# Kernel optimization log

Hardware: AMD Instinct MI355X
Metric: run time of the kernel (lower is better)

The kernel has to match this reference:

```python
import jax, jax.numpy as jnp
import numpy as np

EPS = 1e-5
NUM_CLASSES = 8

def _conv(x, w, b):
    # reflect pad 1 then valid 3x3 conv, NCHW / OIHW
    x = jnp.pad(x, ((0, 0), (0, 0), (1, 1), (1, 1)), mode='reflect')
    y = jax.lax.conv_general_dilated(x, w, (1, 1), 'VALID',
        dimension_numbers=('NCHW', 'OIHW', 'NCHW'))
    return y + b[None, :, None, None]

def _up2(x):
    B, C, H, W = x.shape
    return jax.image.resize(x, (B, C, 2 * H, 2 * W), method='bilinear')

def _nearest_resize_seg(seg, H, W):
    # torch F.interpolate mode='nearest': src = floor(dst * in / out)
    ih = jnp.arange(H) * seg.shape[2] // H
    iw = jnp.arange(W) * seg.shape[3] // W
    return seg[:, :, ih][:, :, :, iw]

def _seg_norm(x, seg):
    # per-class InstanceNorm2d (no affine) on masked copies, summed
    H, W = x.shape[2], x.shape[3]
    seg_r = _nearest_resize_seg(seg, H, W)  # [B,1,H,W]
    out = jnp.zeros_like(x)
    for c in range(NUM_CLASSES):
        mask = (seg_r == c).astype(x.dtype)
        xc = x * mask
        mu = jnp.mean(xc, axis=(2, 3), keepdims=True)
        var = jnp.mean(xc * xc, axis=(2, 3), keepdims=True) - mu * mu
        out = out + (xc - mu) * jax.lax.rsqrt(var + EPS)
    return out

def setup_inputs() -> dict:
    key = jax.random.key(0)
    ks = jax.random.split(key, 24)
    d = {}
    d['x'] = jax.random.normal(ks[0], (4, 512, 64, 64), dtype=jnp.float32)
    d['seg_map'] = jax.random.randint(ks[1], (4, 1, 64, 64), 0, NUM_CLASSES, dtype=jnp.int32)
    shapes = [(256, 512), (256, 256), (256, 256), (256, 256), (128, 256),
              (128, 128), (64, 128), (64, 64), (3, 64)]
    names = ['1', '2', '3', '4', '5', '6', '7', '8', 'f']
    for i, ((o, ic), nm) in enumerate(zip(shapes, names)):
        fan_in = ic * 9
        bound = 1.0 / np.sqrt(fan_in)
        d['w' + nm] = jax.random.uniform(ks[2 + 2 * i], (o, ic, 3, 3), jnp.float32, -bound, bound)
        d['b' + nm] = jax.random.uniform(ks[3 + 2 * i], (o,), jnp.float32, -bound, bound)
    return d

def reference(x, seg_map, w1, b1, w2, b2, w3, b3, w4, b4, w5, b5,
              w6, b6, w7, b7, w8, b8, wf, bf):
    h = jax.nn.relu(_conv(x, w1, b1))
    h = _seg_norm(h, seg_map)
    h = _up2(h)
    h = jax.nn.relu(_conv(h, w2, b2))
    h = jax.nn.relu(_conv(h, w3, b3))
    h = jax.nn.relu(_conv(h, w4, b4))
    h = jax.nn.relu(_conv(h, w5, b5))
    h = _seg_norm(h, seg_map)
    h = _up2(h)
    h = jax.nn.relu(_conv(h, w6, b6))
    h = jax.nn.relu(_conv(h, w7, b7))
    h = _seg_norm(h, seg_map)
    h = _up2(h)
    h = jax.nn.relu(_conv(h, w8, b8))
    return _conv(h, wf, bf)
```

## Files before the change

kernel.cpp:

```cpp
#include <hip/hip_runtime.h>

typedef unsigned int uint;
typedef unsigned short ushort;
typedef __bf16 bf16x8 __attribute__((ext_vector_type(8)));
typedef float f32x4 __attribute__((ext_vector_type(4)));
typedef uint u32x4 __attribute__((ext_vector_type(4)));
typedef ushort u16x4 __attribute__((ext_vector_type(4)));

__device__ __forceinline__ float bf_lo(uint u) { return __builtin_bit_cast(float, u << 16); }
__device__ __forceinline__ float bf_hi(uint u) { return __builtin_bit_cast(float, u & 0xFFFF0000u); }
__device__ __forceinline__ ushort f2bf(float f) {
  uint u = __builtin_bit_cast(uint, f);
  return (ushort)((u + 0x7FFFu + ((u >> 16) & 1u)) >> 16);
}

template<int NCH, int ROWS, int RELU>
__global__ __launch_bounds__(256) void conv_mfma_k(
    const ushort* __restrict__ in, const ushort* __restrict__ wp,
    const float* __restrict__ bias, ushort* __restrict__ out,
    int Cout, int H, int W,
    int in_row0, int in_rows, int out_row0, int out_rows,
    int ob_row0, int ob_rows) {
  constexpr int Cin = NCH * 32;
  constexpr int SLOTS = (ROWS + 2) * 66 * 4;
  constexpr int NPASS = (SLOTS + 255) / 256;
  constexpr int LAST = SLOTS - (NPASS - 1) * 256;
  __shared__ ushort lds[2][SLOTS * 8];
  const int tid = threadIdx.x;
  const int lane = tid & 63;
  const int wv = tid >> 6;
  const int wx0 = blockIdx.x * 64;
  const int nCoB = Cout >> 6;
  const int cob = (blockIdx.z % nCoB) * 64;
  const int b = blockIdx.z / nCoB;
  const int h0 = out_row0 + blockIdx.y * ROWS;
  const int nCb = Cout >> 4;
  const int cb0 = cob >> 4;

  int hs[ROWS + 2];
#pragma unroll
  for (int r = 0; r < ROWS + 2; ++r) {
    int hh = h0 - 1 + r;
    if (hh < 0) hh = 1;
    if (hh >= H) hh = 2 * (H - 1) - hh;
    hh = min(max(hh, in_row0), in_row0 + in_rows - 1);
    hs[r] = hh - in_row0;
  }

  const ushort* gsrc[NPASS];
  uint lof[NPASS];
#pragma unroll
  for (int p = 0; p < NPASS; ++p) {
    const int t = p * 256 + tid;
    const int px_g = t >> 2, kgs = t & 3;
    int rr = px_g / 66;
    int px = px_g - rr * 66;
    if (rr > ROWS + 1) { px = px_g - (ROWS + 2) * 66; rr = ROWS + 1; }
    const int kg = kgs ^ ((px >> 1) & 3);
    int wsrc = wx0 + px - 1;
    wsrc = (wsrc < 0) ? 1 : (wsrc >= W ? W - 2 : wsrc);
    gsrc[p] = in + ((size_t)(b * in_rows + hs[rr]) * W + wsrc) * Cin + kg * 8;
    lof[p] = (uint)((p * 256 + wv * 64) * 8);
  }

  const int bpx = wv * 16 + (lane & 15);
  const int bkg = lane >> 4;

  f32x4 acc[ROWS][4] = {};

  auto stage = [&](int buf, int ci0) {
#pragma unroll
    for (int p = 0; p < NPASS; ++p) {
      if (p + 1 < NPASS || tid < LAST)
        __builtin_amdgcn_global_load_lds(
            (const __attribute__((address_space(1))) void*)(gsrc[p] + ci0),
            (__attribute__((address_space(3))) void*)(&lds[buf][lof[p]]), 16, 0, 0);
    }
  };
  auto compute = [&](int buf, int kc) {
    const ushort* lb = &lds[buf][0];
#pragma unroll
    for (int t9 = 0; t9 < 9; ++t9) {
      const int dr = t9 / 3, s = t9 - dr * 3;
      bf16x8 afr[4];
#pragma unroll
      for (int ii = 0; ii < 4; ++ii) {
        const int off = (((t9 * nCb + cb0 + ii) * NCH + kc) << 9) + (lane << 3);
        afr[ii] = __builtin_bit_cast(bf16x8, *(const u32x4*)(wp + off));
      }
      const int px = bpx + s;
      const int swz = bkg ^ ((px >> 1) & 3);
#pragma unroll
      for (int rr = 0; rr < ROWS; ++rr) {
        const int sl = (((rr + dr) * 66 + px) << 2) + swz;
        const bf16x8 bfrag = __builtin_bit_cast(bf16x8, *(const u32x4*)(lb + sl * 8));
#pragma unroll
        for (int ii = 0; ii < 4; ++ii)
          acc[rr][ii] = __builtin_amdgcn_mfma_f32_16x16x32_bf16(afr[ii], bfrag, acc[rr][ii], 0, 0, 0);
      }
    }
  };

  stage(0, 0);
  asm volatile("s_waitcnt vmcnt(0)" ::: "memory");
  __syncthreads();
#pragma unroll 1
  for (int c = 0; c < NCH; ++c) {
    if (c + 1 < NCH) stage((c + 1) & 1, (c + 1) * 32);
    compute(c & 1, c);
    asm volatile("s_waitcnt vmcnt(0)" ::: "memory");
    __syncthreads();
  }

  const int cofr = cob + (lane >> 4) * 4;
  const int pxo = wx0 + bpx;
#pragma unroll
  for (int rr = 0; rr < ROWS; ++rr) {
    const int h = h0 + rr;
    if (h >= out_row0 + out_rows) break;
    const size_t base = ((size_t)(b * ob_rows + (h - ob_row0)) * W + pxo) * Cout;
#pragma unroll
    for (int ii = 0; ii < 4; ++ii) {
      u16x4 pk;
#pragma unroll
      for (int g = 0; g < 4; ++g) {
        float v = acc[rr][ii][g] + bias[cofr + ii * 16 + g];
        if (RELU) v = fmaxf(v, 0.f);
        pk[g] = f2bf(v);
      }
      *(u16x4*)(out + base + cofr + ii * 16) = pk;
    }
  }
}

__global__ __launch_bounds__(256) void convf_mfma_k(
    const ushort* __restrict__ in, const ushort* __restrict__ wp,
    const float* __restrict__ bias, float* __restrict__ out,
    int in_row0, int in_rows, int out_row0, int out_rows) {
  constexpr int ROWS = 4, NCH = 2, W = 512, H = 512, Cin = 64;
  constexpr int SLOTS = (ROWS + 2) * 66 * 4;
  constexpr int NPASS = (SLOTS + 255) / 256;
  constexpr int LAST = SLOTS - (NPASS - 1) * 256;
  __shared__ ushort lds[2][SLOTS * 8];
  const int tid = threadIdx.x;
  const int lane = tid & 63;
  const int wv = tid >> 6;
  const int wx0 = blockIdx.x * 64;
  const int b = blockIdx.z;
  const int h0 = out_row0 + blockIdx.y * ROWS;

  int hs[ROWS + 2];
#pragma unroll
  for (int r = 0; r < ROWS + 2; ++r) {
    int hh = h0 - 1 + r;
    if (hh < 0) hh = 1;
    if (hh >= H) hh = 2 * (H - 1) - hh;
    hh = min(max(hh, in_row0), in_row0 + in_rows - 1);
    hs[r] = hh - in_row0;
  }
  const ushort* gsrc[NPASS];
  uint lof[NPASS];
#pragma unroll
  for (int p = 0; p < NPASS; ++p) {
    const int t = p * 256 + tid;
    const int px_g = t >> 2, kgs = t & 3;
    int rr = px_g / 66;
    int px = px_g - rr * 66;
    if (rr > ROWS + 1) { px = px_g - (ROWS + 2) * 66; rr = ROWS + 1; }
    const int kg = kgs ^ ((px >> 1) & 3);
    int wsrc = wx0 + px - 1;
    wsrc = (wsrc < 0) ? 1 : (wsrc >= W ? W - 2 : wsrc);
    gsrc[p] = in + ((size_t)(b * in_rows + hs[rr]) * W + wsrc) * Cin + kg * 8;
    lof[p] = (uint)((p * 256 + wv * 64) * 8);
  }
  const int bpx = wv * 16 + (lane & 15);
  const int bkg = lane >> 4;
  f32x4 acc[ROWS] = {};

  auto stage = [&](int buf, int ci0) {
#pragma unroll
    for (int p = 0; p < NPASS; ++p) {
      if (p + 1 < NPASS || tid < LAST)
        __builtin_amdgcn_global_load_lds(
            (const __attribute__((address_space(1))) void*)(gsrc[p] + ci0),
            (__attribute__((address_space(3))) void*)(&lds[buf][lof[p]]), 16, 0, 0);
    }
  };
  auto compute = [&](int buf, int kc) {
    const ushort* lb = &lds[buf][0];
#pragma unroll
    for (int t9 = 0; t9 < 9; ++t9) {
      const int dr = t9 / 3, s = t9 - dr * 3;
      const int off = (((t9 * NCH) + kc) << 9) + (lane << 3);
      const bf16x8 afr = __builtin_bit_cast(bf16x8, *(const u32x4*)(wp + off));
      const int px = bpx + s;
      const int swz = bkg ^ ((px >> 1) & 3);
#pragma unroll
      for (int rr = 0; rr < ROWS; ++rr) {
        const int sl = (((rr + dr) * 66 + px) << 2) + swz;
        const bf16x8 bfrag = __builtin_bit_cast(bf16x8, *(const u32x4*)(lb + sl * 8));
        acc[rr] = __builtin_amdgcn_mfma_f32_16x16x32_bf16(afr, bfrag, acc[rr], 0, 0, 0);
      }
    }
  };

  stage(0, 0);
  asm volatile("s_waitcnt vmcnt(0)" ::: "memory");
  __syncthreads();
#pragma unroll 1
  for (int c = 0; c < NCH; ++c) {
    if (c + 1 < NCH) stage((c + 1) & 1, (c + 1) * 32);
    compute(c & 1, c);
    asm volatile("s_waitcnt vmcnt(0)" ::: "memory");
    __syncthreads();
  }

  if ((lane >> 4) == 0) {
    const int pxo = wx0 + bpx;
#pragma unroll
    for (int rr = 0; rr < ROWS; ++rr) {
      const int h = h0 + rr;
      if (h >= out_row0 + out_rows) break;
#pragma unroll
      for (int g = 0; g < 3; ++g)
        out[(((size_t)(b * 3 + g)) << 18) + ((size_t)h << 9) + pxo] = acc[rr][g] + bias[g];
    }
  }
}

__global__ __launch_bounds__(256) void sn_sum_k(
    const ushort* __restrict__ x, const int* __restrict__ seg,
    float* __restrict__ Ssum, float* __restrict__ Qsum, int C, int logW, int nsl) {
  const int W = 1 << logW, sh = logW - 6;
  const int b = blockIdx.x / nsl, sl = blockIdx.x % nsl;
  const int PPT = 256 / C;
  const int c = threadIdx.x % C;
  const int sub = threadIdx.x / C;
  const int rows = W / nsl;
  const int p0 = sl * rows * W;
  const int np = rows * W;
  const ushort* xp = x + ((size_t)b << (2 * logW)) * C + (size_t)p0 * C;
  const int* segb = seg + (b << 12);
  float S[8] = {0, 0, 0, 0, 0, 0, 0, 0};
  float Q[8] = {0, 0, 0, 0, 0, 0, 0, 0};
  for (int k = sub; k < np; k += PPT) {
    const int p = p0 + k;
    const int cls = segb[(((p >> logW) >> sh) << 6) + ((p & (W - 1)) >> sh)];
    const uint u = xp[(size_t)k * C + c];
    const float v = __builtin_bit_cast(float, u << 16);
#pragma unroll
    for (int t = 0; t < 8; ++t) {
      const bool m = (cls == t);
      S[t] += m ? v : 0.f;
      Q[t] += m ? v * v : 0.f;
    }
  }
#pragma unroll
  for (int t = 0; t < 8; ++t) {
    atomicAdd(&Ssum[((b << 3) + t) * C + c], S[t]);
    atomicAdd(&Qsum[((b << 3) + t) * C + c], Q[t]);
  }
}

__global__ void sn_fin_k(const float* __restrict__ Ssum, const float* __restrict__ Qsum,
                         float* __restrict__ RS, float* __restrict__ KK, int C, float invN) {
  const int tid = threadIdx.x;
  const int b = tid / C, c = tid % C;
  float K = 0.f;
#pragma unroll
  for (int t = 0; t < 8; ++t) {
    const float s = Ssum[((b << 3) + t) * C + c];
    const float q = Qsum[((b << 3) + t) * C + c];
    const float mu = s * invN;
    const float var = q * invN - mu * mu;
    const float r = rsqrtf(var + 1e-5f);
    RS[((b << 3) + t) * C + c] = r;
    K += mu * r;
  }
  KK[b * C + c] = K;
}

__global__ __launch_bounds__(256) void up2norm_k(
    const ushort* __restrict__ src, const int* __restrict__ seg,
    const float* __restrict__ RS, const float* __restrict__ KK,
    ushort* __restrict__ out, int C, int logWs, int out_row0, int out_rows) {
  const int Ws = 1 << logWs, W2 = Ws << 1, sh = logWs - 6;
  const int cpb = C >> 3;
  int i = blockIdx.x * 256 + threadIdx.x;
  const int total = 4 * out_rows * W2 * cpb;
  if (i >= total) return;
  const int cc = (i % cpb) * 8; i /= cpb;
  const int ow = i % W2; i /= W2;
  const int r = i % out_rows;
  const int b = i / out_rows;
  const int oh = out_row0 + r;

  int hl = (oh - 1) >> 1;
  const float hf = (oh & 1) ? 0.25f : 0.75f;
  const int hh = min(hl + 1, Ws - 1);
  hl = max(hl, 0);
  int wl = (ow - 1) >> 1;
  const float wfc = (ow & 1) ? 0.25f : 0.75f;
  const int wh = min(wl + 1, Ws - 1);
  wl = max(wl, 0);

  const size_t pl = (size_t)b << (2 * logWs);
  const u32x4 xll = *(const u32x4*)(src + ((pl + hl * Ws + wl) * C + cc));
  const u32x4 xlh = *(const u32x4*)(src + ((pl + hl * Ws + wh) * C + cc));
  const u32x4 xhl = *(const u32x4*)(src + ((pl + hh * Ws + wl) * C + cc));
  const u32x4 xhh = *(const u32x4*)(src + ((pl + hh * Ws + wh) * C + cc));
  const int* segb = seg + (b << 12);
  const int cll = segb[((hl >> sh) << 6) + (wl >> sh)];
  const int clh = segb[((hl >> sh) << 6) + (wh >> sh)];
  const int chl = segb[((hh >> sh) << 6) + (wl >> sh)];
  const int chh = segb[((hh >> sh) << 6) + (wh >> sh)];
  const float* rll = RS + ((b << 3) + cll) * C + cc;
  const float* rlh = RS + ((b << 3) + clh) * C + cc;
  const float* rhl = RS + ((b << 3) + chl) * C + cc;
  const float* rhh = RS + ((b << 3) + chh) * C + cc;
  const float* kk = KK + b * C + cc;

  u32x4 res;
#pragma unroll
  for (int q = 0; q < 4; ++q) {
    const int c0 = 2 * q, c1 = 2 * q + 1;
    const float na0 = bf_lo(xll[q]) * rll[c0], nb0 = bf_lo(xlh[q]) * rlh[c0];
    const float nc0 = bf_lo(xhl[q]) * rhl[c0], nd0 = bf_lo(xhh[q]) * rhh[c0];
    const float na1 = bf_hi(xll[q]) * rll[c1], nb1 = bf_hi(xlh[q]) * rlh[c1];
    const float nc1 = bf_hi(xhl[q]) * rhl[c1], nd1 = bf_hi(xhh[q]) * rhh[c1];
    const float t0 = na0 + wfc * (nb0 - na0), bo0 = nc0 + wfc * (nd0 - nc0);
    const float t1 = na1 + wfc * (nb1 - na1), bo1 = nc1 + wfc * (nd1 - nc1);
    const float o0 = t0 + hf * (bo0 - t0) - kk[c0];
    const float o1 = t1 + hf * (bo1 - t1) - kk[c1];
    res[q] = (uint)f2bf(o0) | ((uint)f2bf(o1) << 16);
  }
  *(u32x4*)(out + (((size_t)(b * out_rows + r)) * W2 + ow) * C + cc) = res;
}

__global__ __launch_bounds__(256) void packw_k(const float* __restrict__ w,
                                               ushort* __restrict__ wp, int Co, int Ci) {
  const int i = blockIdx.x * 256 + threadIdx.x;
  const int tot = Co * Ci * 9;
  if (i >= tot) return;
  const int nKc = Ci >> 5;
  const int nCb = Co >> 4;
  const int j = i & 7;
  const int l = (i >> 3) & 63;
  int rest = i >> 9;
  const int kc = rest % nKc; rest /= nKc;
  const int cb = rest % nCb;
  const int t9 = rest / nCb;
  const int co = cb * 16 + (l & 15);
  const int ci = kc * 32 + (l >> 4) * 8 + j;
  wp[i] = f2bf(w[((size_t)(co * Ci + ci)) * 9 + t9]);
}

__global__ __launch_bounds__(256) void packwf_k(const float* __restrict__ w,
                                                ushort* __restrict__ wp) {
  const int i = blockIdx.x * 256 + threadIdx.x;
  if (i >= 9216) return;
  const int j = i & 7;
  const int l = (i >> 3) & 63;
  const int rest = i >> 9;
  const int kc = rest & 1;
  const int t9 = rest >> 1;
  const int co = l & 15;
  const int ci = kc * 32 + (l >> 4) * 8 + j;
  wp[i] = (co < 3) ? f2bf(w[((size_t)(co * 64 + ci)) * 9 + t9]) : (ushort)0;
}

__global__ __launch_bounds__(256) void cvt_x_k(const float* __restrict__ x,
                                               ushort* __restrict__ xn) {
  __shared__ float tile[32][65];
  const int p0 = blockIdx.x * 64, c0 = blockIdx.y * 32, b = blockIdx.z;
  for (int k = threadIdx.x; k < 2048; k += 256) {
    const int ci = k >> 6, pj = k & 63;
    tile[ci][pj] = x[(((size_t)(b * 512 + c0 + ci)) << 12) + p0 + pj];
  }
  __syncthreads();
  for (int k = threadIdx.x; k < 2048; k += 256) {
    const int ci = k & 31, pj = k >> 5;
    xn[((((size_t)b << 12) + p0 + pj)) * 512 + c0 + ci] = f2bf(tile[ci][pj]);
  }
}

extern "C" void kernel_launch(void* const* d_in, const int* in_sizes, int n_in,
                              void* d_out, int out_size, void* d_ws, size_t ws_size,
                              hipStream_t stream) {
  const float* x = (const float*)d_in[0];
  const int* seg = (const int*)d_in[1];
  const float *w1 = (const float*)d_in[2], *b1 = (const float*)d_in[3];
  const float *w2 = (const float*)d_in[4], *b2 = (const float*)d_in[5];
  const float *w3 = (const float*)d_in[6], *b3 = (const float*)d_in[7];
  const float *w4 = (const float*)d_in[8], *b4 = (const float*)d_in[9];
  const float *w5 = (const float*)d_in[10], *b5 = (const float*)d_in[11];
  const float *w6 = (const float*)d_in[12], *b6 = (const float*)d_in[13];
  const float *w7 = (const float*)d_in[14], *b7 = (const float*)d_in[15];
  const float *w8 = (const float*)d_in[16], *b8 = (const float*)d_in[17];
  const float *wf = (const float*)d_in[18], *bf = (const float*)d_in[19];
  float* outp = (float*)d_out;

  char* wsb = (char*)d_ws;
  const size_t MB = 1048576;
  ushort* w1p = (ushort*)(wsb + 0);
  ushort* w2p = (ushort*)(wsb + 2359296);
  ushort* w3p = (ushort*)(wsb + 3538944);
  ushort* w4p = (ushort*)(wsb + 4718592);
  ushort* w5p = (ushort*)(wsb + 5898240);
  ushort* w6p = (ushort*)(wsb + 6488064);
  ushort* w7p = (ushort*)(wsb + 6782976);
  ushort* w8p = (ushort*)(wsb + 6930432);
  ushort* wfp = (ushort*)(wsb + 7004160);
  float* Ssum = (float*)(wsb + 8388608);
  float* Qsum = (float*)(wsb + 8421376);
  float* RS = (float*)(wsb + 8454144);
  float* KK = (float*)(wsb + 8486912);
  ushort* XN = (ushort*)(wsb + 9 * MB);
  ushort* A1 = (ushort*)(wsb + 25 * MB);
  ushort* U1 = (ushort*)(wsb + 33 * MB);
  ushort* C2 = (ushort*)(wsb + 65 * MB);
  ushort* C3 = (ushort*)(wsb + 9 * MB);
  ushort* C4 = (ushort*)(wsb + 41 * MB);
  ushort* C5 = (ushort*)(wsb + 9 * MB);
  ushort* U6 = (ushort*)(wsb + 25 * MB);
  ushort* C6 = (ushort*)(wsb + 58 * MB);
  ushort* C7 = (ushort*)(wsb + 91 * MB);
  ushort* U8 = (ushort*)(wsb + 9 * MB);
  ushort* C8 = (ushort*)(wsb + 43 * MB);

  auto cdiv = [](int a, int b) { return (a + b - 1) / b; };

  cvt_x_k<<<dim3(64, 16, 4), 256, 0, stream>>>(x, XN);
  packw_k<<<cdiv(1179648, 256), 256, 0, stream>>>(w1, w1p, 256, 512);
  packw_k<<<cdiv(589824, 256), 256, 0, stream>>>(w2, w2p, 256, 256);
  packw_k<<<cdiv(589824, 256), 256, 0, stream>>>(w3, w3p, 256, 256);
  packw_k<<<cdiv(589824, 256), 256, 0, stream>>>(w4, w4p, 256, 256);
  packw_k<<<cdiv(294912, 256), 256, 0, stream>>>(w5, w5p, 128, 256);
  packw_k<<<cdiv(147456, 256), 256, 0, stream>>>(w6, w6p, 128, 128);
  packw_k<<<cdiv(73728, 256), 256, 0, stream>>>(w7, w7p, 64, 128);
  packw_k<<<cdiv(36864, 256), 256, 0, stream>>>(w8, w8p, 64, 64);
  packwf_k<<<36, 256, 0, stream>>>(wf, wfp);

  conv_mfma_k<16, 2, 1><<<dim3(1, 32, 16), 256, 0, stream>>>(
      XN, w1p, b1, A1, 256, 64, 64, 0, 64, 0, 64, 0, 64);
  hipMemsetAsync(Ssum, 0, 65536, stream);
  sn_sum_k<<<4 * 32, 256, 0, stream>>>(A1, seg, Ssum, Qsum, 256, 6, 32);
  sn_fin_k<<<1, 1024, 0, stream>>>(Ssum, Qsum, RS, KK, 256, 1.f / 4096.f);
  up2norm_k<<<cdiv(4 * 128 * 128 * 32, 256), 256, 0, stream>>>(A1, seg, RS, KK, U1, 256, 6, 0, 128);

  conv_mfma_k<8, 4, 1><<<dim3(2, 32, 16), 256, 0, stream>>>(
      U1, w2p, b2, C2, 256, 128, 128, 0, 128, 0, 128, 0, 128);
  conv_mfma_k<8, 4, 1><<<dim3(2, 32, 16), 256, 0, stream>>>(
      C2, w3p, b3, C3, 256, 128, 128, 0, 128, 0, 128, 0, 128);
  conv_mfma_k<8, 4, 1><<<dim3(2, 32, 16), 256, 0, stream>>>(
      C3, w4p, b4, C4, 256, 128, 128, 0, 128, 0, 128, 0, 128);
  conv_mfma_k<8, 4, 1><<<dim3(2, 32, 8), 256, 0, stream>>>(
      C4, w5p, b5, C5, 128, 128, 128, 0, 128, 0, 128, 0, 128);
  hipMemsetAsync(Ssum, 0, 65536, stream);
  sn_sum_k<<<4 * 64, 256, 0, stream>>>(C5, seg, Ssum, Qsum, 128, 7, 64);
  sn_fin_k<<<1, 512, 0, stream>>>(Ssum, Qsum, RS, KK, 128, 1.f / 16384.f);

  for (int kb = 0; kb < 2; ++kb) {
    const int r0 = kb * 128;
    const int Rlo = max(r0 - 1, 0), Rhi = min(r0 + 128, 255);
    const int rows6 = Rhi - Rlo + 1;
    const int Ulo = max(Rlo - 1, 0), Uhi = min(Rhi + 1, 255);
    const int rowsU = Uhi - Ulo + 1;
    up2norm_k<<<cdiv(4 * rowsU * 256 * 16, 256), 256, 0, stream>>>(C5, seg, RS, KK, U6, 128, 7, Ulo, rowsU);
    conv_mfma_k<4, 4, 1><<<dim3(4, cdiv(rows6, 4), 8), 256, 0, stream>>>(
        U6, w6p, b6, C6, 128, 256, 256, Ulo, rowsU, Rlo, rows6, Rlo, rows6);
    conv_mfma_k<4, 4, 1><<<dim3(4, 32, 4), 256, 0, stream>>>(
        C6, w7p, b7, C7, 64, 256, 256, Rlo, rows6, r0, 128, 0, 256);
  }
  hipMemsetAsync(Ssum, 0, 65536, stream);
  sn_sum_k<<<4 * 128, 256, 0, stream>>>(C7, seg, Ssum, Qsum, 64, 8, 128);
  sn_fin_k<<<1, 256, 0, stream>>>(Ssum, Qsum, RS, KK, 64, 1.f / 65536.f);

  for (int kb = 0; kb < 4; ++kb) {
    const int r0 = kb * 128;
    const int Rlo = max(r0 - 1, 0), Rhi = min(r0 + 128, 511);
    const int rows8 = Rhi - Rlo + 1;
    const int Ulo = max(Rlo - 1, 0), Uhi = min(Rhi + 1, 511);
    const int rowsU = Uhi - Ulo + 1;
    up2norm_k<<<cdiv(4 * rowsU * 512 * 8, 256), 256, 0, stream>>>(C7, seg, RS, KK, U8, 64, 8, Ulo, rowsU);
    conv_mfma_k<2, 4, 1><<<dim3(8, cdiv(rows8, 4), 4), 256, 0, stream>>>(
        U8, w8p, b8, C8, 64, 512, 512, Ulo, rowsU, Rlo, rows8, Rlo, rows8);
    convf_mfma_k<<<dim3(8, 32, 4), 256, 0, stream>>>(C8, wfp, bf, outp, Rlo, rows8, r0, 128);
  }
}
```

Before: 1.228 ms.

## Software-pipeline conv fragment loads across taps and merge weight packing launches

Inside the MFMA conv kernels, the weight and LDS fragments for the next 3x3 tap are loaded into a second register buffer while MFMAs run on the current tap. The global-to-LDS staging of the next channel chunk is now issued after compute instead of before it. The eight weight-packing launches are merged into one kernel that walks a segment table. Together these aim to hide load latency and cut launch overhead, but the double buffering raises register use, and issuing the stage after compute shortens the window in which that global load can overlap with MFMA work.

```diff
diff --git a/kernel.cpp b/kernel.cpp
--- a/kernel.cpp
+++ b/kernel.cpp
@@ -79,24 +79,40 @@
   };
   auto compute = [&](int buf, int kc) {
     const ushort* lb = &lds[buf][0];
+    u32x4 afr[2][4];
+    u32x4 bfr[2][ROWS];
+#pragma unroll
+    for (int ii = 0; ii < 4; ++ii)
+      afr[0][ii] = *(const u32x4*)(wp + ((((0 * nCb + cb0 + ii) * NCH + kc) << 9) + (lane << 3)));
+    {
+      const int px = bpx;
+      const int swz = bkg ^ ((px >> 1) & 3);
+#pragma unroll
+      for (int rr = 0; rr < ROWS; ++rr)
+        bfr[0][rr] = *(const u32x4*)(lb + (((rr * 66 + px) << 2) + swz) * 8);
+    }
 #pragma unroll
     for (int t9 = 0; t9 < 9; ++t9) {
-      const int dr = t9 / 3, s = t9 - dr * 3;
-      bf16x8 afr[4];
-#pragma unroll
-      for (int ii = 0; ii < 4; ++ii) {
-        const int off = (((t9 * nCb + cb0 + ii) * NCH + kc) << 9) + (lane << 3);
-        afr[ii] = __builtin_bit_cast(bf16x8, *(const u32x4*)(wp + off));
+      const int cur = t9 & 1, nxt = cur ^ 1;
+      if (t9 < 8) {
+        const int tn = t9 + 1;
+        const int drn = tn / 3, sn = tn - drn * 3;
+#pragma unroll
+        for (int ii = 0; ii < 4; ++ii)
+          afr[nxt][ii] = *(const u32x4*)(wp + ((((tn * nCb + cb0 + ii) * NCH + kc) << 9) + (lane << 3)));
+        const int pxn = bpx + sn;
+        const int swzn = bkg ^ ((pxn >> 1) & 3);
+#pragma unroll
+        for (int rr = 0; rr < ROWS; ++rr)
+          bfr[nxt][rr] = *(const u32x4*)(lb + ((((rr + drn) * 66 + pxn) << 2) + swzn) * 8);
       }
-      const int px = bpx + s;
-      const int swz = bkg ^ ((px >> 1) & 3);
 #pragma unroll
       for (int rr = 0; rr < ROWS; ++rr) {
-        const int sl = (((rr + dr) * 66 + px) << 2) + swz;
-        const bf16x8 bfrag = __builtin_bit_cast(bf16x8, *(const u32x4*)(lb + sl * 8));
+        const bf16x8 bb = __builtin_bit_cast(bf16x8, bfr[cur][rr]);
 #pragma unroll
         for (int ii = 0; ii < 4; ++ii)
-          acc[rr][ii] = __builtin_amdgcn_mfma_f32_16x16x32_bf16(afr[ii], bfrag, acc[rr][ii], 0, 0, 0);
+          acc[rr][ii] = __builtin_amdgcn_mfma_f32_16x16x32_bf16(
+              __builtin_bit_cast(bf16x8, afr[cur][ii]), bb, acc[rr][ii], 0, 0, 0);
       }
     }
   };
@@ -106,8 +122,8 @@
   __syncthreads();
 #pragma unroll 1
   for (int c = 0; c < NCH; ++c) {
+    compute(c & 1, c);
     if (c + 1 < NCH) stage((c + 1) & 1, (c + 1) * 32);
-    compute(c & 1, c);
     asm volatile("s_waitcnt vmcnt(0)" ::: "memory");
     __syncthreads();
   }
@@ -188,19 +204,34 @@
   };
   auto compute = [&](int buf, int kc) {
     const ushort* lb = &lds[buf][0];
+    u32x4 afr[2];
+    u32x4 bfr[2][ROWS];
+    afr[0] = *(const u32x4*)(wp + (((0 * NCH + kc) << 9) + (lane << 3)));
+    {
+      const int px = bpx;
+      const int swz = bkg ^ ((px >> 1) & 3);
+#pragma unroll
+      for (int rr = 0; rr < ROWS; ++rr)
+        bfr[0][rr] = *(const u32x4*)(lb + (((rr * 66 + px) << 2) + swz) * 8);
+    }
 #pragma unroll
     for (int t9 = 0; t9 < 9; ++t9) {
-      const int dr = t9 / 3, s = t9 - dr * 3;
-      const int off = (((t9 * NCH) + kc) << 9) + (lane << 3);
-      const bf16x8 afr = __builtin_bit_cast(bf16x8, *(const u32x4*)(wp + off));
-      const int px = bpx + s;
-      const int swz = bkg ^ ((px >> 1) & 3);
-#pragma unroll
-      for (int rr = 0; rr < ROWS; ++rr) {
-        const int sl = (((rr + dr) * 66 + px) << 2) + swz;
-        const bf16x8 bfrag = __builtin_bit_cast(bf16x8, *(const u32x4*)(lb + sl * 8));
-        acc[rr] = __builtin_amdgcn_mfma_f32_16x16x32_bf16(afr, bfrag, acc[rr], 0, 0, 0);
+      const int cur = t9 & 1, nxt = cur ^ 1;
+      if (t9 < 8) {
+        const int tn = t9 + 1;
+        const int drn = tn / 3, sn = tn - drn * 3;
+        afr[nxt] = *(const u32x4*)(wp + (((tn * NCH + kc) << 9) + (lane << 3)));
+        const int pxn = bpx + sn;
+        const int swzn = bkg ^ ((pxn >> 1) & 3);
+#pragma unroll
+        for (int rr = 0; rr < ROWS; ++rr)
+          bfr[nxt][rr] = *(const u32x4*)(lb + ((((rr + drn) * 66 + pxn) << 2) + swzn) * 8);
       }
+#pragma unroll
+      for (int rr = 0; rr < ROWS; ++rr)
+        acc[rr] = __builtin_amdgcn_mfma_f32_16x16x32_bf16(
+            __builtin_bit_cast(bf16x8, afr[cur]),
+            __builtin_bit_cast(bf16x8, bfr[cur][rr]), acc[rr], 0, 0, 0);
     }
   };
 
@@ -209,8 +240,8 @@
   __syncthreads();
 #pragma unroll 1
   for (int c = 0; c < NCH; ++c) {
+    compute(c & 1, c);
     if (c + 1 < NCH) stage((c + 1) & 1, (c + 1) * 32);
-    compute(c & 1, c);
     asm volatile("s_waitcnt vmcnt(0)" ::: "memory");
     __syncthreads();
   }
@@ -337,22 +368,28 @@
   *(u32x4*)(out + (((size_t)(b * out_rows + r)) * W2 + ow) * C + cc) = res;
 }
 
-__global__ __launch_bounds__(256) void packw_k(const float* __restrict__ w,
-                                               ushort* __restrict__ wp, int Co, int Ci) {
-  const int i = blockIdx.x * 256 + threadIdx.x;
-  const int tot = Co * Ci * 9;
-  if (i >= tot) return;
-  const int nKc = Ci >> 5;
-  const int nCb = Co >> 4;
-  const int j = i & 7;
-  const int l = (i >> 3) & 63;
-  int rest = i >> 9;
-  const int kc = rest % nKc; rest /= nKc;
-  const int cb = rest % nCb;
-  const int t9 = rest / nCb;
-  const int co = cb * 16 + (l & 15);
-  const int ci = kc * 32 + (l >> 4) * 8 + j;
-  wp[i] = f2bf(w[((size_t)(co * Ci + ci)) * 9 + t9]);
+struct PWSeg { const float* w; ushort* p; int Co, Ci; };
+struct PackArgs { PWSeg s[8]; };
+__global__ __launch_bounds__(256) void packall_k(PackArgs a) {
+  int i = blockIdx.x * 256 + threadIdx.x;
+#pragma unroll
+  for (int k = 0; k < 8; ++k) {
+    const int Co = a.s[k].Co, Ci = a.s[k].Ci;
+    const int tot = Co * Ci * 9;
+    if (i < tot) {
+      const int nKc = Ci >> 5, nCb = Co >> 4;
+      const int j = i & 7, l = (i >> 3) & 63;
+      int rest = i >> 9;
+      const int kc = rest % nKc; rest /= nKc;
+      const int cb = rest % nCb;
+      const int t9 = rest / nCb;
+      const int co = cb * 16 + (l & 15);
+      const int ci = kc * 32 + (l >> 4) * 8 + j;
+      a.s[k].p[i] = f2bf(a.s[k].w[((size_t)(co * Ci + ci)) * 9 + t9]);
+      return;
+    }
+    i -= tot;
+  }
 }
 
 __global__ __launch_bounds__(256) void packwf_k(const float* __restrict__ w,
@@ -431,14 +468,16 @@
   auto cdiv = [](int a, int b) { return (a + b - 1) / b; };
 
   cvt_x_k<<<dim3(64, 16, 4), 256, 0, stream>>>(x, XN);
-  packw_k<<<cdiv(1179648, 256), 256, 0, stream>>>(w1, w1p, 256, 512);
-  packw_k<<<cdiv(589824, 256), 256, 0, stream>>>(w2, w2p, 256, 256);
-  packw_k<<<cdiv(589824, 256), 256, 0, stream>>>(w3, w3p, 256, 256);
-  packw_k<<<cdiv(589824, 256), 256, 0, stream>>>(w4, w4p, 256, 256);
-  packw_k<<<cdiv(294912, 256), 256, 0, stream>>>(w5, w5p, 128, 256);
-  packw_k<<<cdiv(147456, 256), 256, 0, stream>>>(w6, w6p, 128, 128);
-  packw_k<<<cdiv(73728, 256), 256, 0, stream>>>(w7, w7p, 64, 128);
-  packw_k<<<cdiv(36864, 256), 256, 0, stream>>>(w8, w8p, 64, 64);
+  PackArgs pa;
+  pa.s[0] = {w1, w1p, 256, 512};
+  pa.s[1] = {w2, w2p, 256, 256};
+  pa.s[2] = {w3, w3p, 256, 256};
+  pa.s[3] = {w4, w4p, 256, 256};
+  pa.s[4] = {w5, w5p, 128, 256};
+  pa.s[5] = {w6, w6p, 128, 128};
+  pa.s[6] = {w7, w7p, 64, 128};
+  pa.s[7] = {w8, w8p, 64, 64};
+  packall_k<<<cdiv(3502080, 256), 256, 0, stream>>>(pa);
   packwf_k<<<36, 256, 0, stream>>>(wf, wfp);
 
   conv_mfma_k<16, 2, 1><<<dim3(1, 32, 16), 256, 0, stream>>>(
```

Result: slower. 1.254 ms (+2.1%).
